# Kernel optimization log

Hardware: AMD Instinct MI355X
Metric: run time of the kernel (lower is better)

Reference implementation:

```python
import jax, jax.numpy as jnp
import numpy as np

B, C, H, W = 16, 256, 32, 32
NUM_HEADS = 8
GN_GROUPS = 8
GN_EPS = 1e-5


def setup_inputs() -> dict:
    key = jax.random.key(0)
    k1, k2, k3 = jax.random.split(key, 3)
    x = jax.random.normal(k1, (B, C, H, W), dtype=jnp.float32)
    # 1x1 convs == channel matmuls; store weights as [out_ch, in_ch]
    w_qkv = jax.random.normal(k2, (3 * C, C), dtype=jnp.float32) * (C ** -0.5)
    w_proj = jax.random.normal(k3, (C, C), dtype=jnp.float32) * (C ** -0.5)
    gn_gamma = jnp.ones((C,), dtype=jnp.float32)
    gn_beta = jnp.zeros((C,), dtype=jnp.float32)
    return {"x": x, "w_qkv": w_qkv, "w_proj": w_proj, "gn_gamma": gn_gamma, "gn_beta": gn_beta}


def reference(x, w_qkv, w_proj, gn_gamma, gn_beta):
    b, c, h, w = x.shape
    nh = NUM_HEADS
    hd = c // nh
    hw = h * w
    residual = x

    # qkv 1x1 conv (no bias): [b,3c,h,w]
    qkv = jnp.einsum('oc,bchw->bohw', w_qkv, x)
    # reshape(b,3,nh,hd,hw) then permute(1,0,2,4,3) -> (3,b,nh,hw,hd)
    qkv = qkv.reshape(b, 3, nh, hd, hw).transpose(1, 0, 2, 4, 3)
    q, k, v = qkv[0], qkv[1], qkv[2]  # each [b,nh,hw,hd]

    scale = hd ** -0.5
    attn = jnp.einsum('bnid,bnjd->bnij', q, k) * scale  # [b,nh,hw,hw]
    attn = attn - jnp.max(attn, axis=-1, keepdims=True)
    attn = jax.nn.softmax(attn, axis=-1)
    out = jnp.einsum('bnij,bnjd->bnid', attn, v)  # [b,nh,hw,hd]

    # permute(0,1,3,2) -> [b,nh,hd,hw] -> [b,c,h,w]
    out = out.transpose(0, 1, 3, 2).reshape(b, c, h, w)

    # proj 1x1 conv
    out = jnp.einsum('oc,bchw->bohw', w_proj, out)

    # GroupNorm(8, c)
    g = GN_GROUPS
    og = out.reshape(b, g, c // g, h, w)
    mean = jnp.mean(og, axis=(2, 3, 4), keepdims=True)
    var = jnp.var(og, axis=(2, 3, 4), keepdims=True)
    og = (og - mean) * jax.lax.rsqrt(var + GN_EPS)
    out = og.reshape(b, c, h, w) * gn_gamma[None, :, None, None] + gn_beta[None, :, None, None]

    return out + residual
```

## Files before the change

### kernel.cpp

```cpp
#include <hip/hip_runtime.h>
#include <hip/hip_bf16.h>
#include <math.h>

#define BATCH 16
#define CCH 256
#define HW 1024
#define NH 8
#define HD 32
#define SCALE 0.17677669529663687f

typedef __attribute__((ext_vector_type(8))) short bf16x8;
typedef __attribute__((ext_vector_type(4))) short bf16x4;
typedef __attribute__((ext_vector_type(4))) float f32x4;

__device__ __forceinline__ unsigned short bf16bits(float f) {
  __hip_bfloat16 h = __float2bfloat16(f);
  return *(unsigned short*)&h;
}

__device__ __forceinline__ void gload16(const void* g, void* l) {
  __builtin_amdgcn_global_load_lds(
      (const __attribute__((address_space(1))) unsigned int*)g,
      (__attribute__((address_space(3))) unsigned int*)l, 16, 0, 0);
}

__global__ __launch_bounds__(256) void cvt_w(const float* __restrict__ w,
                                             unsigned short* __restrict__ wb, int n4) {
  int i = blockIdx.x * 256 + threadIdx.x;
  if (i >= n4) return;
  float4 v = ((const float4*)w)[i];
  ushort4 o;
  o.x = bf16bits(v.x); o.y = bf16bits(v.y); o.z = bf16bits(v.z); o.w = bf16bits(v.w);
  ((ushort4*)wb)[i] = o;
}

__global__ __launch_bounds__(256) void cvt_x(const float* __restrict__ x,
                                             unsigned short* __restrict__ xt) {
  __shared__ unsigned short tile[64][72];
  const int t = threadIdx.x;
  const int p0 = blockIdx.x * 64;
  const int c0 = blockIdx.y * 64;
  const int b = blockIdx.z;
  const float* xb = x + (size_t)b * CCH * HW;
#pragma unroll
  for (int i = 0; i < 4; ++i) {
    int f = i * 256 + t;
    int c = f >> 4, p4 = f & 15;
    float4 v = *(const float4*)(xb + (size_t)(c0 + c) * HW + p0 + p4 * 4);
    tile[p4 * 4 + 0][c] = bf16bits(v.x);
    tile[p4 * 4 + 1][c] = bf16bits(v.y);
    tile[p4 * 4 + 2][c] = bf16bits(v.z);
    tile[p4 * 4 + 3][c] = bf16bits(v.w);
  }
  __syncthreads();
  unsigned short* xtb = xt + (size_t)b * HW * CCH;
#pragma unroll
  for (int i = 0; i < 4; ++i) {
    int f = i * 256 + t;
    int p = f >> 4, c4 = f & 15;
    ushort4 v = *(const ushort4*)&tile[p][c4 * 4];
    *(ushort4*)(xtb + (size_t)(p0 + p) * CCH + c0 + c4 * 4) = v;
  }
}

__global__ __launch_bounds__(256) void qkv_mfma(const unsigned short* __restrict__ Wb,
                                                const unsigned short* __restrict__ Xt,
                                                unsigned short* __restrict__ Qb,
                                                unsigned short* __restrict__ Kf,
                                                unsigned short* __restrict__ Vf) {
  __shared__ unsigned short A_l[8 * 128 * 8];
  __shared__ unsigned short B_l[8 * 128 * 8];
  const int t = threadIdx.x;
  const int wave = t >> 6, lane = t & 63;
  const int quad = lane >> 4, n16 = lane & 15;
  const int o0 = blockIdx.x * 128;
  const int p0 = blockIdx.y * 128;
  const int b = blockIdx.z;
  const int wm = (wave >> 1) * 64, wn = (wave & 1) * 64;
  const unsigned short* Xb = Xt + (size_t)b * (HW * CCH);

  f32x4 acc[4][4] = {};
  for (int k0 = 0; k0 < CCH; k0 += 64) {
#pragma unroll
    for (int i = 0; i < 4; ++i) {
      int f = i * 256 + t;
      int kc = f >> 7, m = f & 127;
      int dst = (i * 256 + wave * 64) * 8;
      gload16(Wb + (size_t)(o0 + m) * CCH + k0 + kc * 8, &A_l[dst]);
      gload16(Xb + (size_t)(p0 + m) * CCH + k0 + kc * 8, &B_l[dst]);
    }
    __syncthreads();
#pragma unroll
    for (int ks = 0; ks < 2; ++ks) {
      bf16x8 af[4], bfr[4];
#pragma unroll
      for (int mi = 0; mi < 4; ++mi)
        af[mi] = *(const bf16x8*)&A_l[((ks * 4 + quad) * 128 + wm + mi * 16 + n16) * 8];
#pragma unroll
      for (int ni = 0; ni < 4; ++ni)
        bfr[ni] = *(const bf16x8*)&B_l[((ks * 4 + quad) * 128 + wn + ni * 16 + n16) * 8];
#pragma unroll
      for (int mi = 0; mi < 4; ++mi)
#pragma unroll
        for (int ni = 0; ni < 4; ++ni)
          acc[mi][ni] = __builtin_amdgcn_mfma_f32_16x16x32_bf16(af[mi], bfr[ni], acc[mi][ni], 0, 0, 0);
    }
    __syncthreads();
  }
  const int three = o0 >> 8;
#pragma unroll
  for (int mi = 0; mi < 4; ++mi) {
    int o = o0 + wm + mi * 16 + quad * 4;
    int head = (o >> 5) & 7;
    int d0 = (mi & 1) * 16 + quad * 4;
    size_t bh64 = (size_t)(b * NH + head) * 64;
    size_t bh_base = (size_t)(b * NH + head) * (HW * HD);
#pragma unroll
    for (int ni = 0; ni < 4; ++ni) {
      int p = p0 + wn + ni * 16 + n16;
      if (three == 0) {
        ushort4 st;
        st.x = bf16bits(acc[mi][ni][0] * SCALE);
        st.y = bf16bits(acc[mi][ni][1] * SCALE);
        st.z = bf16bits(acc[mi][ni][2] * SCALE);
        st.w = bf16bits(acc[mi][ni][3] * SCALE);
        *(ushort4*)&Qb[bh_base + (size_t)p * HD + d0] = st;
      } else if (three == 1) {
        int kb = p >> 4;
        size_t chunk = (bh64 + kb) * 64 + (d0 >> 3) * 16 + n16;
        ushort4 st;
        st.x = bf16bits(acc[mi][ni][0]);
        st.y = bf16bits(acc[mi][ni][1]);
        st.z = bf16bits(acc[mi][ni][2]);
        st.w = bf16bits(acc[mi][ni][3]);
        *(ushort4*)&Kf[chunk * 8 + (d0 & 7)] = st;
      } else {
        int kb = p >> 4;
        size_t base = (bh64 + kb) * 64 + (n16 >> 2) * 16 + quad * 4;
#pragma unroll
        for (int r = 0; r < 4; ++r)
          Vf[(base + r) * 8 + (mi & 1) * 4 + (n16 & 3)] = bf16bits(acc[mi][ni][r]);
      }
    }
  }
}

__global__ __launch_bounds__(256) void attn_mfma(const unsigned short* __restrict__ Q,
                                                 const unsigned short* __restrict__ Kf,
                                                 const unsigned short* __restrict__ Vf,
                                                 unsigned short* __restrict__ Ab) {
  __shared__ unsigned short Ksh[4 * 64 * 8];
  __shared__ unsigned short Vsh[4 * 64 * 8];
  const int t = threadIdx.x;
  const int lane = t & 63;
  const int quad = lane >> 4, n16 = lane & 15;
  const int wave = t >> 6;
  const int id = blockIdx.y * 16 + blockIdx.x;
  const int xcd = id & 7, jj = id >> 3;
  const int bh = xcd * 16 + (jj >> 4);
  const int qtile = jj & 15;
  const int i0w = qtile * 64 + wave * 16;
  const size_t hb = (size_t)bh * (HW * HD);
  const size_t fb = (size_t)bh * 64 * 64 * 8;

  bf16x8 qf = *(const bf16x8*)((const short*)Q + hb + (size_t)(i0w + n16) * HD + quad * 8);
  f32x4 O00 = {0.f, 0.f, 0.f, 0.f}, O01 = {0.f, 0.f, 0.f, 0.f};
  f32x4 O10 = {0.f, 0.f, 0.f, 0.f}, O11 = {0.f, 0.f, 0.f, 0.f};
  const f32x4 zero = {0.f, 0.f, 0.f, 0.f};
  float l_lane = 0.f;

  for (int jt = 0; jt < 16; ++jt) {
    gload16(Kf + fb + ((size_t)jt * 4 * 64 + t) * 8, &Ksh[t * 8]);
    gload16(Vf + fb + ((size_t)jt * 4 * 64 + t) * 8, &Vsh[t * 8]);
    __syncthreads();
    f32x4 S[4];
#pragma unroll
    for (int kk = 0; kk < 4; ++kk) {
      bf16x8 kfr = *(const bf16x8*)&Ksh[(kk * 64 + lane) * 8];
      S[kk] = __builtin_amdgcn_mfma_f32_16x16x32_bf16(kfr, qf, zero, 0, 0, 0);
    }
    bf16x4 pfA[4];
#pragma unroll
    for (int kk = 0; kk < 4; ++kk) {
      float e0 = __expf(S[kk][0]);
      float e1 = __expf(S[kk][1]);
      float e2 = __expf(S[kk][2]);
      float e3 = __expf(S[kk][3]);
      l_lane += (e0 + e1) + (e2 + e3);
      bf16x4 p4;
      p4[0] = (short)bf16bits(e0); p4[1] = (short)bf16bits(e1);
      p4[2] = (short)bf16bits(e2); p4[3] = (short)bf16bits(e3);
      pfA[kk] = p4;
    }
#pragma unroll
    for (int kk = 0; kk < 4; ++kk) {
      bf16x8 vv = *(const bf16x8*)&Vsh[(kk * 64 + lane) * 8];
      bf16x4 v0 = __builtin_shufflevector(vv, vv, 0, 1, 2, 3);
      bf16x4 v1 = __builtin_shufflevector(vv, vv, 4, 5, 6, 7);
      if (kk & 1) {
        O01 = __builtin_amdgcn_mfma_f32_16x16x16bf16_1k(pfA[kk], v0, O01, 0, 0, 0);
        O11 = __builtin_amdgcn_mfma_f32_16x16x16bf16_1k(pfA[kk], v1, O11, 0, 0, 0);
      } else {
        O00 = __builtin_amdgcn_mfma_f32_16x16x16bf16_1k(pfA[kk], v0, O00, 0, 0, 0);
        O10 = __builtin_amdgcn_mfma_f32_16x16x16bf16_1k(pfA[kk], v1, O10, 0, 0, 0);
      }
    }
    __syncthreads();
  }
  f32x4 O0, O1;
#pragma unroll
  for (int r = 0; r < 4; ++r) { O0[r] = O00[r] + O01[r]; O1[r] = O10[r] + O11[r]; }
  l_lane += __shfl_xor(l_lane, 16, 64);
  l_lane += __shfl_xor(l_lane, 32, 64);
  float linv = 1.f / l_lane;
  float lq[4];
#pragma unroll
  for (int r = 0; r < 4; ++r) lq[r] = __shfl(linv, quad * 4 + r, 64);
  const int bb = bh >> 3, head = bh & 7;
  unsigned short* dst = Ab + (size_t)bb * (HW * CCH) + head * 32;
#pragma unroll
  for (int r = 0; r < 4; ++r) {
    int p = i0w + quad * 4 + r;
    dst[(size_t)p * CCH + n16] = bf16bits(O0[r] * lq[r]);
    dst[(size_t)p * CCH + 16 + n16] = bf16bits(O1[r] * lq[r]);
  }
}

__global__ __launch_bounds__(256) void proj_mfma(const unsigned short* __restrict__ Wb,
                                                 const unsigned short* __restrict__ At,
                                                 float* __restrict__ P) {
  __shared__ unsigned short A_l[8 * 128 * 8];
  __shared__ unsigned short B_l[8 * 128 * 8];
  const int t = threadIdx.x;
  const int wave = t >> 6, lane = t & 63;
  const int quad = lane >> 4, n16 = lane & 15;
  const int o0 = blockIdx.x * 128;
  const int p0 = blockIdx.y * 128;
  const int b = blockIdx.z;
  const int wm = (wave >> 1) * 64, wn = (wave & 1) * 64;
  const unsigned short* Ax = At + (size_t)b * (HW * CCH);

  f32x4 acc[4][4] = {};
  for (int k0 = 0; k0 < CCH; k0 += 64) {
#pragma unroll
    for (int i = 0; i < 4; ++i) {
      int f = i * 256 + t;
      int kc = f >> 7, m = f & 127;
      int dst = (i * 256 + wave * 64) * 8;
      gload16(Wb + (size_t)(o0 + m) * CCH + k0 + kc * 8, &A_l[dst]);
      gload16(Ax + (size_t)(p0 + m) * CCH + k0 + kc * 8, &B_l[dst]);
    }
    __syncthreads();
#pragma unroll
    for (int ks = 0; ks < 2; ++ks) {
      bf16x8 af[4], bfr[4];
#pragma unroll
      for (int mi = 0; mi < 4; ++mi)
        af[mi] = *(const bf16x8*)&A_l[((ks * 4 + quad) * 128 + wm + mi * 16 + n16) * 8];
#pragma unroll
      for (int ni = 0; ni < 4; ++ni)
        bfr[ni] = *(const bf16x8*)&B_l[((ks * 4 + quad) * 128 + wn + ni * 16 + n16) * 8];
#pragma unroll
      for (int mi = 0; mi < 4; ++mi)
#pragma unroll
        for (int ni = 0; ni < 4; ++ni)
          acc[mi][ni] = __builtin_amdgcn_mfma_f32_16x16x32_bf16(af[mi], bfr[ni], acc[mi][ni], 0, 0, 0);
    }
    __syncthreads();
  }
#pragma unroll
  for (int mi = 0; mi < 4; ++mi) {
    int o = o0 + wm + mi * 16 + quad * 4;
#pragma unroll
    for (int ni = 0; ni < 4; ++ni) {
      int p = p0 + wn + ni * 16 + n16;
#pragma unroll
      for (int r = 0; r < 4; ++r)
        P[(size_t)b * (CCH * HW) + (size_t)(o + r) * HW + p] = acc[mi][ni][r];
    }
  }
}

__global__ __launch_bounds__(256) void gn_stats(const float* __restrict__ P,
                                                float* __restrict__ stats) {
  __shared__ float r1[256], r2[256];
  const int t = threadIdx.x;
  const int bg = blockIdx.x;
  const float4* Pg = (const float4*)(P + (size_t)bg * 32768);
  float s1 = 0.f, s2 = 0.f;
  for (int idx = t; idx < 8192; idx += 256) {
    float4 v = Pg[idx];
    s1 += v.x + v.y + v.z + v.w;
    s2 += v.x * v.x + v.y * v.y + v.z * v.z + v.w * v.w;
  }
  r1[t] = s1; r2[t] = s2;
  __syncthreads();
  for (int off = 128; off > 0; off >>= 1) {
    if (t < off) { r1[t] += r1[t + off]; r2[t] += r2[t + off]; }
    __syncthreads();
  }
  if (t == 0) {
    float mean = r1[0] * (1.f / 32768.f);
    float var = r2[0] * (1.f / 32768.f) - mean * mean;
    stats[bg * 2] = mean;
    stats[bg * 2 + 1] = rsqrtf(var + 1e-5f);
  }
}

__global__ __launch_bounds__(256) void gn_apply(const float* __restrict__ P,
                                                const float* __restrict__ x,
                                                const float* __restrict__ gamma,
                                                const float* __restrict__ beta,
                                                const float* __restrict__ stats,
                                                float* __restrict__ out) {
  int i4 = blockIdx.x * 256 + threadIdx.x;
  int c = (i4 >> 8) & 255;
  int bg = i4 >> 13;
  float mean = stats[bg * 2];
  float inv = stats[bg * 2 + 1];
  float ga = gamma[c] * inv;
  float be = beta[c] - mean * ga;
  float4 p = ((const float4*)P)[i4];
  float4 xr = ((const float4*)x)[i4];
  float4 o;
  o.x = p.x * ga + be + xr.x;
  o.y = p.y * ga + be + xr.y;
  o.z = p.z * ga + be + xr.z;
  o.w = p.w * ga + be + xr.w;
  ((float4*)out)[i4] = o;
}

extern "C" void kernel_launch(void* const* d_in, const int* in_sizes, int n_in,
                              void* d_out, int out_size, void* d_ws, size_t ws_size,
                              hipStream_t stream) {
  const float* x      = (const float*)d_in[0];
  const float* w_qkv  = (const float*)d_in[1];
  const float* w_proj = (const float*)d_in[2];
  const float* gamma  = (const float*)d_in[3];
  const float* beta   = (const float*)d_in[4];
  float* out = (float*)d_out;

  const size_t SZ = (size_t)BATCH * CCH * HW;
  float* P = (float*)d_ws;
  float* stats = P + SZ;
  unsigned short* Qb  = (unsigned short*)(stats + 256);
  unsigned short* Kfr = Qb + SZ;
  unsigned short* Vfr = Kfr + SZ;
  unsigned short* Ab  = Vfr + SZ;
  unsigned short* Xtb = Ab + SZ;
  unsigned short* Wqb = Xtb + SZ;
  unsigned short* Wpb = Wqb + (3 * CCH * CCH);

  cvt_w<<<192, 256, 0, stream>>>(w_qkv, Wqb, 3 * CCH * CCH / 4);
  cvt_w<<<64, 256, 0, stream>>>(w_proj, Wpb, CCH * CCH / 4);
  cvt_x<<<dim3(16, 4, BATCH), 256, 0, stream>>>(x, Xtb);
  qkv_mfma<<<dim3(6, 8, BATCH), 256, 0, stream>>>(Wqb, Xtb, Qb, Kfr, Vfr);
  attn_mfma<<<dim3(16, 128), 256, 0, stream>>>(Qb, Kfr, Vfr, Ab);
  proj_mfma<<<dim3(2, 8, BATCH), 256, 0, stream>>>(Wpb, Ab, P);
  gn_stats<<<128, 256, 0, stream>>>(P, stats);
  gn_apply<<<4096, 256, 0, stream>>>(P, x, gamma, beta, stats, out);
}
```

Before: 169.7 us.

## Fuse GroupNorm stats into proj, store bf16 proj output, widen attention tiles

Several changes at once. Q is pre-scaled by log2(e)/sqrt(d) so softmax can use the hardware exp2, and probabilities are packed to bf16 by truncation with a byte permute. Each attention wave now handles 32 query rows, so every K/V tile loaded into LDS is reused twice and the grid is halved. Proj now writes bf16 output and accumulates GroupNorm sums through wave reductions and atomics, which removes the separate stats kernel and halves the traffic into gn_apply, at the cost of extra rounding error and a small zeroing launch.

```diff
diff --git a/kernel.cpp b/kernel.cpp
--- a/kernel.cpp
+++ b/kernel.cpp
@@ -7,7 +7,7 @@
 #define HW 1024
 #define NH 8
 #define HD 32
-#define SCALE 0.17677669529663687f
+#define QSCALE 0.25500526954123462f
 
 typedef __attribute__((ext_vector_type(8))) short bf16x8;
 typedef __attribute__((ext_vector_type(4))) short bf16x4;
@@ -22,6 +22,10 @@
   __builtin_amdgcn_global_load_lds(
       (const __attribute__((address_space(1))) unsigned int*)g,
       (__attribute__((address_space(3))) unsigned int*)l, 16, 0, 0);
+}
+
+__device__ __forceinline__ unsigned int pack_bf16_trunc(float a, float b) {
+  return __builtin_amdgcn_perm(__float_as_uint(b), __float_as_uint(a), 0x07060302u);
 }
 
 __global__ __launch_bounds__(256) void cvt_w(const float* __restrict__ w,
@@ -32,6 +36,10 @@
   ushort4 o;
   o.x = bf16bits(v.x); o.y = bf16bits(v.y); o.z = bf16bits(v.z); o.w = bf16bits(v.w);
   ((ushort4*)wb)[i] = o;
+}
+
+__global__ __launch_bounds__(256) void zero_stats(float* __restrict__ gstats) {
+  gstats[threadIdx.x] = 0.f;
 }
 
 __global__ __launch_bounds__(256) void cvt_x(const float* __restrict__ x,
@@ -120,10 +128,10 @@
       int p = p0 + wn + ni * 16 + n16;
       if (three == 0) {
         ushort4 st;
-        st.x = bf16bits(acc[mi][ni][0] * SCALE);
-        st.y = bf16bits(acc[mi][ni][1] * SCALE);
-        st.z = bf16bits(acc[mi][ni][2] * SCALE);
-        st.w = bf16bits(acc[mi][ni][3] * SCALE);
+        st.x = bf16bits(acc[mi][ni][0] * QSCALE);
+        st.y = bf16bits(acc[mi][ni][1] * QSCALE);
+        st.z = bf16bits(acc[mi][ni][2] * QSCALE);
+        st.w = bf16bits(acc[mi][ni][3] * QSCALE);
         *(ushort4*)&Qb[bh_base + (size_t)p * HD + d0] = st;
       } else if (three == 1) {
         int kb = p >> 4;
@@ -155,42 +163,53 @@
   const int lane = t & 63;
   const int quad = lane >> 4, n16 = lane & 15;
   const int wave = t >> 6;
-  const int id = blockIdx.y * 16 + blockIdx.x;
+  const int id = blockIdx.y * 8 + blockIdx.x;
   const int xcd = id & 7, jj = id >> 3;
-  const int bh = xcd * 16 + (jj >> 4);
-  const int qtile = jj & 15;
-  const int i0w = qtile * 64 + wave * 16;
+  const int bh = xcd * 16 + (jj >> 3);
+  const int qtile = jj & 7;
+  const int i0w = qtile * 128 + wave * 32;
   const size_t hb = (size_t)bh * (HW * HD);
   const size_t fb = (size_t)bh * 64 * 64 * 8;
 
-  bf16x8 qf = *(const bf16x8*)((const short*)Q + hb + (size_t)(i0w + n16) * HD + quad * 8);
-  f32x4 O00 = {0.f, 0.f, 0.f, 0.f}, O01 = {0.f, 0.f, 0.f, 0.f};
-  f32x4 O10 = {0.f, 0.f, 0.f, 0.f}, O11 = {0.f, 0.f, 0.f, 0.f};
+  bf16x8 qf0 = *(const bf16x8*)((const short*)Q + hb + (size_t)(i0w + n16) * HD + quad * 8);
+  bf16x8 qf1 = *(const bf16x8*)((const short*)Q + hb + (size_t)(i0w + 16 + n16) * HD + quad * 8);
+  f32x4 O000 = {0,0,0,0}, O001 = {0,0,0,0}, O010 = {0,0,0,0}, O011 = {0,0,0,0};
+  f32x4 O100 = {0,0,0,0}, O101 = {0,0,0,0}, O110 = {0,0,0,0}, O111 = {0,0,0,0};
   const f32x4 zero = {0.f, 0.f, 0.f, 0.f};
-  float l_lane = 0.f;
+  float l0 = 0.f, l1 = 0.f;
 
   for (int jt = 0; jt < 16; ++jt) {
     gload16(Kf + fb + ((size_t)jt * 4 * 64 + t) * 8, &Ksh[t * 8]);
     gload16(Vf + fb + ((size_t)jt * 4 * 64 + t) * 8, &Vsh[t * 8]);
     __syncthreads();
-    f32x4 S[4];
+    f32x4 S0[4], S1[4];
 #pragma unroll
     for (int kk = 0; kk < 4; ++kk) {
       bf16x8 kfr = *(const bf16x8*)&Ksh[(kk * 64 + lane) * 8];
-      S[kk] = __builtin_amdgcn_mfma_f32_16x16x32_bf16(kfr, qf, zero, 0, 0, 0);
-    }
-    bf16x4 pfA[4];
+      S0[kk] = __builtin_amdgcn_mfma_f32_16x16x32_bf16(kfr, qf0, zero, 0, 0, 0);
+      S1[kk] = __builtin_amdgcn_mfma_f32_16x16x32_bf16(kfr, qf1, zero, 0, 0, 0);
+    }
+    bf16x4 pf0[4], pf1[4];
 #pragma unroll
     for (int kk = 0; kk < 4; ++kk) {
-      float e0 = __expf(S[kk][0]);
-      float e1 = __expf(S[kk][1]);
-      float e2 = __expf(S[kk][2]);
-      float e3 = __expf(S[kk][3]);
-      l_lane += (e0 + e1) + (e2 + e3);
-      bf16x4 p4;
-      p4[0] = (short)bf16bits(e0); p4[1] = (short)bf16bits(e1);
-      p4[2] = (short)bf16bits(e2); p4[3] = (short)bf16bits(e3);
-      pfA[kk] = p4;
+      float a0 = __builtin_amdgcn_exp2f(S0[kk][0]);
+      float a1 = __builtin_amdgcn_exp2f(S0[kk][1]);
+      float a2 = __builtin_amdgcn_exp2f(S0[kk][2]);
+      float a3 = __builtin_amdgcn_exp2f(S0[kk][3]);
+      l0 += (a0 + a1) + (a2 + a3);
+      unsigned int plo = pack_bf16_trunc(a0, a1);
+      unsigned int phi = pack_bf16_trunc(a2, a3);
+      unsigned int* pw = (unsigned int*)&pf0[kk];
+      pw[0] = plo; pw[1] = phi;
+      float b0 = __builtin_amdgcn_exp2f(S1[kk][0]);
+      float b1 = __builtin_amdgcn_exp2f(S1[kk][1]);
+      float b2 = __builtin_amdgcn_exp2f(S1[kk][2]);
+      float b3 = __builtin_amdgcn_exp2f(S1[kk][3]);
+      l1 += (b0 + b1) + (b2 + b3);
+      unsigned int qlo = pack_bf16_trunc(b0, b1);
+      unsigned int qhi = pack_bf16_trunc(b2, b3);
+      unsigned int* qw = (unsigned int*)&pf1[kk];
+      qw[0] = qlo; qw[1] = qhi;
     }
 #pragma unroll
     for (int kk = 0; kk < 4; ++kk) {
@@ -198,37 +217,51 @@
       bf16x4 v0 = __builtin_shufflevector(vv, vv, 0, 1, 2, 3);
       bf16x4 v1 = __builtin_shufflevector(vv, vv, 4, 5, 6, 7);
       if (kk & 1) {
-        O01 = __builtin_amdgcn_mfma_f32_16x16x16bf16_1k(pfA[kk], v0, O01, 0, 0, 0);
-        O11 = __builtin_amdgcn_mfma_f32_16x16x16bf16_1k(pfA[kk], v1, O11, 0, 0, 0);
+        O001 = __builtin_amdgcn_mfma_f32_16x16x16bf16_1k(pf0[kk], v0, O001, 0, 0, 0);
+        O011 = __builtin_amdgcn_mfma_f32_16x16x16bf16_1k(pf0[kk], v1, O011, 0, 0, 0);
+        O101 = __builtin_amdgcn_mfma_f32_16x16x16bf16_1k(pf1[kk], v0, O101, 0, 0, 0);
+        O111 = __builtin_amdgcn_mfma_f32_16x16x16bf16_1k(pf1[kk], v1, O111, 0, 0, 0);
       } else {
-        O00 = __builtin_amdgcn_mfma_f32_16x16x16bf16_1k(pfA[kk], v0, O00, 0, 0, 0);
-        O10 = __builtin_amdgcn_mfma_f32_16x16x16bf16_1k(pfA[kk], v1, O10, 0, 0, 0);
+        O000 = __builtin_amdgcn_mfma_f32_16x16x16bf16_1k(pf0[kk], v0, O000, 0, 0, 0);
+        O010 = __builtin_amdgcn_mfma_f32_16x16x16bf16_1k(pf0[kk], v1, O010, 0, 0, 0);
+        O100 = __builtin_amdgcn_mfma_f32_16x16x16bf16_1k(pf1[kk], v0, O100, 0, 0, 0);
+        O110 = __builtin_amdgcn_mfma_f32_16x16x16bf16_1k(pf1[kk], v1, O110, 0, 0, 0);
       }
     }
     __syncthreads();
   }
-  f32x4 O0, O1;
-#pragma unroll
-  for (int r = 0; r < 4; ++r) { O0[r] = O00[r] + O01[r]; O1[r] = O10[r] + O11[r]; }
-  l_lane += __shfl_xor(l_lane, 16, 64);
-  l_lane += __shfl_xor(l_lane, 32, 64);
-  float linv = 1.f / l_lane;
-  float lq[4];
-#pragma unroll
-  for (int r = 0; r < 4; ++r) lq[r] = __shfl(linv, quad * 4 + r, 64);
+  f32x4 A0, A1, B0, B1;
+#pragma unroll
+  for (int r = 0; r < 4; ++r) {
+    A0[r] = O000[r] + O001[r]; A1[r] = O010[r] + O011[r];
+    B0[r] = O100[r] + O101[r]; B1[r] = O110[r] + O111[r];
+  }
+  l0 += __shfl_xor(l0, 16, 64); l0 += __shfl_xor(l0, 32, 64);
+  l1 += __shfl_xor(l1, 16, 64); l1 += __shfl_xor(l1, 32, 64);
+  float linv0 = 1.f / l0, linv1 = 1.f / l1;
+  float lq0[4], lq1[4];
+#pragma unroll
+  for (int r = 0; r < 4; ++r) {
+    lq0[r] = __shfl(linv0, quad * 4 + r, 64);
+    lq1[r] = __shfl(linv1, quad * 4 + r, 64);
+  }
   const int bb = bh >> 3, head = bh & 7;
   unsigned short* dst = Ab + (size_t)bb * (HW * CCH) + head * 32;
 #pragma unroll
   for (int r = 0; r < 4; ++r) {
-    int p = i0w + quad * 4 + r;
-    dst[(size_t)p * CCH + n16] = bf16bits(O0[r] * lq[r]);
-    dst[(size_t)p * CCH + 16 + n16] = bf16bits(O1[r] * lq[r]);
+    int p0r = i0w + quad * 4 + r;
+    dst[(size_t)p0r * CCH + n16] = bf16bits(A0[r] * lq0[r]);
+    dst[(size_t)p0r * CCH + 16 + n16] = bf16bits(A1[r] * lq0[r]);
+    int p1r = i0w + 16 + quad * 4 + r;
+    dst[(size_t)p1r * CCH + n16] = bf16bits(B0[r] * lq1[r]);
+    dst[(size_t)p1r * CCH + 16 + n16] = bf16bits(B1[r] * lq1[r]);
   }
 }
 
 __global__ __launch_bounds__(256) void proj_mfma(const unsigned short* __restrict__ Wb,
                                                  const unsigned short* __restrict__ At,
-                                                 float* __restrict__ P) {
+                                                 unsigned short* __restrict__ Pb,
+                                                 float* __restrict__ gstats) {
   __shared__ unsigned short A_l[8 * 128 * 8];
   __shared__ unsigned short B_l[8 * 128 * 8];
   const int t = threadIdx.x;
@@ -270,63 +303,53 @@
   }
 #pragma unroll
   for (int mi = 0; mi < 4; ++mi) {
-    int o = o0 + wm + mi * 16 + quad * 4;
+    int obase = o0 + wm + mi * 16;
+    int o = obase + quad * 4;
+    float s1 = 0.f, s2 = 0.f;
 #pragma unroll
     for (int ni = 0; ni < 4; ++ni) {
       int p = p0 + wn + ni * 16 + n16;
 #pragma unroll
-      for (int r = 0; r < 4; ++r)
-        P[(size_t)b * (CCH * HW) + (size_t)(o + r) * HW + p] = acc[mi][ni][r];
-    }
-  }
-}
-
-__global__ __launch_bounds__(256) void gn_stats(const float* __restrict__ P,
-                                                float* __restrict__ stats) {
-  __shared__ float r1[256], r2[256];
-  const int t = threadIdx.x;
-  const int bg = blockIdx.x;
-  const float4* Pg = (const float4*)(P + (size_t)bg * 32768);
-  float s1 = 0.f, s2 = 0.f;
-  for (int idx = t; idx < 8192; idx += 256) {
-    float4 v = Pg[idx];
-    s1 += v.x + v.y + v.z + v.w;
-    s2 += v.x * v.x + v.y * v.y + v.z * v.z + v.w * v.w;
-  }
-  r1[t] = s1; r2[t] = s2;
-  __syncthreads();
-  for (int off = 128; off > 0; off >>= 1) {
-    if (t < off) { r1[t] += r1[t + off]; r2[t] += r2[t + off]; }
-    __syncthreads();
-  }
-  if (t == 0) {
-    float mean = r1[0] * (1.f / 32768.f);
-    float var = r2[0] * (1.f / 32768.f) - mean * mean;
-    stats[bg * 2] = mean;
-    stats[bg * 2 + 1] = rsqrtf(var + 1e-5f);
-  }
-}
-
-__global__ __launch_bounds__(256) void gn_apply(const float* __restrict__ P,
+      for (int r = 0; r < 4; ++r) {
+        float v = acc[mi][ni][r];
+        s1 += v; s2 += v * v;
+        Pb[(size_t)b * (CCH * HW) + (size_t)(o + r) * HW + p] = bf16bits(v);
+      }
+    }
+#pragma unroll
+    for (int m = 1; m < 64; m <<= 1) {
+      s1 += __shfl_xor(s1, m, 64);
+      s2 += __shfl_xor(s2, m, 64);
+    }
+    if (lane == 0) {
+      int bg = b * 8 + (obase >> 5);
+      atomicAdd(&gstats[bg * 2], s1);
+      atomicAdd(&gstats[bg * 2 + 1], s2);
+    }
+  }
+}
+
+__global__ __launch_bounds__(256) void gn_apply(const unsigned short* __restrict__ Pb,
                                                 const float* __restrict__ x,
                                                 const float* __restrict__ gamma,
                                                 const float* __restrict__ beta,
-                                                const float* __restrict__ stats,
+                                                const float* __restrict__ gstats,
                                                 float* __restrict__ out) {
   int i4 = blockIdx.x * 256 + threadIdx.x;
   int c = (i4 >> 8) & 255;
   int bg = i4 >> 13;
-  float mean = stats[bg * 2];
-  float inv = stats[bg * 2 + 1];
+  float mean = gstats[bg * 2] * (1.f / 32768.f);
+  float var = gstats[bg * 2 + 1] * (1.f / 32768.f) - mean * mean;
+  float inv = rsqrtf(var + 1e-5f);
   float ga = gamma[c] * inv;
   float be = beta[c] - mean * ga;
-  float4 p = ((const float4*)P)[i4];
+  ushort4 pu = ((const ushort4*)Pb)[i4];
   float4 xr = ((const float4*)x)[i4];
   float4 o;
-  o.x = p.x * ga + be + xr.x;
-  o.y = p.y * ga + be + xr.y;
-  o.z = p.z * ga + be + xr.z;
-  o.w = p.w * ga + be + xr.w;
+  o.x = __uint_as_float((unsigned)pu.x << 16) * ga + be + xr.x;
+  o.y = __uint_as_float((unsigned)pu.y << 16) * ga + be + xr.y;
+  o.z = __uint_as_float((unsigned)pu.z << 16) * ga + be + xr.z;
+  o.w = __uint_as_float((unsigned)pu.w << 16) * ga + be + xr.w;
   ((float4*)out)[i4] = o;
 }
 
@@ -341,22 +364,22 @@
   float* out = (float*)d_out;
 
   const size_t SZ = (size_t)BATCH * CCH * HW;
-  float* P = (float*)d_ws;
-  float* stats = P + SZ;
-  unsigned short* Qb  = (unsigned short*)(stats + 256);
+  unsigned short* Pb = (unsigned short*)d_ws;
+  unsigned short* Qb  = Pb + SZ;
   unsigned short* Kfr = Qb + SZ;
   unsigned short* Vfr = Kfr + SZ;
   unsigned short* Ab  = Vfr + SZ;
   unsigned short* Xtb = Ab + SZ;
   unsigned short* Wqb = Xtb + SZ;
   unsigned short* Wpb = Wqb + (3 * CCH * CCH);
+  float* gstats = (float*)(Wpb + CCH * CCH);
 
   cvt_w<<<192, 256, 0, stream>>>(w_qkv, Wqb, 3 * CCH * CCH / 4);
   cvt_w<<<64, 256, 0, stream>>>(w_proj, Wpb, CCH * CCH / 4);
+  zero_stats<<<1, 256, 0, stream>>>(gstats);
   cvt_x<<<dim3(16, 4, BATCH), 256, 0, stream>>>(x, Xtb);
   qkv_mfma<<<dim3(6, 8, BATCH), 256, 0, stream>>>(Wqb, Xtb, Qb, Kfr, Vfr);
-  attn_mfma<<<dim3(16, 128), 256, 0, stream>>>(Qb, Kfr, Vfr, Ab);
-  proj_mfma<<<dim3(2, 8, BATCH), 256, 0, stream>>>(Wpb, Ab, P);
-  gn_stats<<<128, 256, 0, stream>>>(P, stats);
-  gn_apply<<<4096, 256, 0, stream>>>(P, x, gamma, beta, stats, out);
-}
+  attn_mfma<<<dim3(8, 128), 256, 0, stream>>>(Qb, Kfr, Vfr, Ab);
+  proj_mfma<<<dim3(2, 8, BATCH), 256, 0, stream>>>(Wpb, Ab, Pb, gstats);
+  gn_apply<<<4096, 256, 0, stream>>>(Pb, x, gamma, beta, gstats, out);
+}
```

Measured after the change: 217.7 us. +28.3%, slower.
